# Kernel optimization log

Measured on AMD Instinct MI355X. Metric: run time of the kernel, lower is better.

Reference implementation:

```python
import jax, jax.numpy as jnp
import numpy as np

N = 100000
E = 1600000
G = 2048
D = 128
F_IN = 9
BN_EPS = 1e-5


def setup_inputs() -> dict:
    key = jax.random.key(0)
    ks = jax.random.split(key, 20)
    def glorot(k, shape):
        lim = float(np.sqrt(6.0 / (shape[0] + shape[1])))
        return jax.random.uniform(k, shape, jnp.float32, -lim, lim)
    inp = {
        'x': jax.random.normal(ks[0], (N, F_IN), jnp.float32),
        'edge_index': jax.random.randint(ks[1], (2, E), 0, N, jnp.int64),
        'batch_index': jnp.sort(jax.random.randint(ks[2], (N,), 0, G, jnp.int64)),
        'W0': glorot(ks[3], (F_IN, D)), 'b0': jnp.zeros((D,), jnp.float32),
        'W1': glorot(ks[4], (D, D)), 'b1': jnp.zeros((D,), jnp.float32),
        'W2': glorot(ks[5], (D, D)), 'b2': jnp.zeros((D,), jnp.float32),
        'W3': glorot(ks[6], (D, D)), 'b3': jnp.zeros((D,), jnp.float32),
        'g1': jnp.ones((D,), jnp.float32), 'be1': jnp.zeros((D,), jnp.float32),
        'g2': jnp.ones((D,), jnp.float32), 'be2': jnp.zeros((D,), jnp.float32),
        'g3': jnp.ones((D,), jnp.float32), 'be3': jnp.zeros((D,), jnp.float32),
        'Wout': glorot(ks[7], (D, 1)), 'bout': jnp.zeros((1,), jnp.float32),
    }
    return inp


def _gcn_conv(x, W, b, row, col, dinv):
    # PyG GCNConv: out = D^-1/2 (A+I) D^-1/2 (x W) + b
    lin = x @ W                                  # [N, D]
    coef = (dinv[row] * dinv[col])[:, None]      # [E, 1]
    agg = jax.ops.segment_sum(lin[row] * coef, col, num_segments=N)
    agg = agg + (dinv * dinv)[:, None] * lin     # self-loop term
    return agg + b


def _bn(x, gamma, beta):
    # BatchNorm1d training-mode: batch stats over node dim, biased variance
    m = jnp.mean(x, axis=0)
    v = jnp.var(x, axis=0)
    return (x - m) * jax.lax.rsqrt(v + BN_EPS) * gamma + beta


def reference(x, edge_index, batch_index, W0, b0, W1, b1, W2, b2, W3, b3,
              g1, be1, g2, be2, g3, be3, Wout, bout):
    row, col = edge_index[0], edge_index[1]
    # degrees with self-loops (all edge weights = 1)
    deg = jax.ops.segment_sum(jnp.ones((E,), x.dtype), col, num_segments=N) + 1.0
    dinv = jax.lax.rsqrt(deg)
    lrelu = lambda h: jax.nn.leaky_relu(h, negative_slope=0.01)

    h = _bn(lrelu(_gcn_conv(x, W0, b0, row, col, dinv)), g1, be1)
    h = _bn(lrelu(_gcn_conv(h, W1, b1, row, col, dinv)), g2, be2)
    h = _bn(lrelu(_gcn_conv(h, W2, b2, row, col, dinv)), g3, be3)
    h = lrelu(_gcn_conv(h, W3, b3, row, col, dinv))

    # global mean pool over graphs
    sums = jax.ops.segment_sum(h, batch_index, num_segments=G)
    cnts = jax.ops.segment_sum(jnp.ones((N,), x.dtype), batch_index, num_segments=G)
    pooled = sums / jnp.maximum(cnts, 1.0)[:, None]   # [G, D]
    return pooled @ Wout + bout                       # [G, 1]
```

## Files before the change

kernel.cpp:

```cpp
#include <hip/hip_runtime.h>


#define LRELU(z) ((z) > 0.f ? (z) : 0.01f * (z))
#define ADD4(d, s) \
  { d.x += s.x; d.y += s.y; d.z += s.z; d.w += s.w; }

typedef __attribute__((ext_vector_type(8))) short short8;
typedef __attribute__((ext_vector_type(4))) float float4v;

__device__ inline unsigned bf16_rn(float a) {
  unsigned u = __float_as_uint(a);
  return (u + 0x7FFFu + ((u >> 16) & 1u)) >> 16;
}

__device__ inline unsigned pack_bf16x2(float a, float b) {
  return bf16_rn(a) | (bf16_rn(b) << 16);
}

__device__ inline float bf16f(unsigned short s) {
  return __uint_as_float(((unsigned)s) << 16);
}

__device__ inline float4 unpack_bf16x4(uint2 u) {
  float4 r;
  r.x = __uint_as_float(u.x << 16);
  r.y = __uint_as_float(u.x & 0xffff0000u);
  r.z = __uint_as_float(u.y << 16);
  r.w = __uint_as_float(u.y & 0xffff0000u);
  return r;
}

__global__ __launch_bounds__(256) void k_count(const int* __restrict__ ei,
                                               int* __restrict__ cnt,
                                               int* __restrict__ rank, int E) {
  int i = blockIdx.x * 256 + threadIdx.x;
  if (i < E) rank[i] = atomicAdd(&cnt[ei[E + i]], 1);
}

__global__ __launch_bounds__(256) void k_scan1(const int* __restrict__ cnt,
                                               int* __restrict__ incl,
                                               int* __restrict__ bsums,
                                               float* __restrict__ dinv, int N) {
  __shared__ int s[256];
  int tid = threadIdx.x;
  int idx = blockIdx.x * 256 + tid;
  int v = (idx < N) ? cnt[idx] : 0;
  if (idx < N) dinv[idx] = rsqrtf((float)(v + 1));
  s[tid] = v;
  __syncthreads();
  for (int off = 1; off < 256; off <<= 1) {
    int t = (tid >= off) ? s[tid - off] : 0;
    __syncthreads();
    s[tid] += t;
    __syncthreads();
  }
  if (idx < N) incl[idx] = s[tid];
  if (tid == 255) bsums[blockIdx.x] = s[255];
}

__global__ __launch_bounds__(512) void k_scan2(const int* __restrict__ bsums,
                                               int* __restrict__ bpref, int nb) {
  __shared__ int s[512];
  int tid = threadIdx.x;
  int v = (tid < nb) ? bsums[tid] : 0;
  s[tid] = v;
  __syncthreads();
  for (int off = 1; off < 512; off <<= 1) {
    int t = (tid >= off) ? s[tid - off] : 0;
    __syncthreads();
    s[tid] += t;
    __syncthreads();
  }
  bpref[tid] = s[tid] - v;
}

__global__ __launch_bounds__(256) void k_cntg(const int* __restrict__ batch,
                                              float* __restrict__ cntG,
                                              int N, int G) {
  int g = blockIdx.x * 256 + threadIdx.x;
  if (g >= G) return;
  int lo = 0, hi = N;
  while (lo < hi) { int mid = (lo + hi) >> 1; if (batch[mid] < g) lo = mid + 1; else hi = mid; }
  int a = lo;
  hi = N;
  while (lo < hi) { int mid = (lo + hi) >> 1; if (batch[mid] < g + 1) lo = mid + 1; else hi = mid; }
  cntG[g] = (float)(lo - a);
}

__global__ __launch_bounds__(256) void k_scan3_prep(
    const int* __restrict__ incl, const int* __restrict__ cnt,
    const int* __restrict__ bpref, int* __restrict__ offs,
    int2* __restrict__ meta, const float* __restrict__ x,
    const float* __restrict__ dinv, unsigned* __restrict__ u, int N) {
  int idx = blockIdx.x * 256 + threadIdx.x;
  if (idx >= N) return;
  int c = cnt[idx];
  int off = incl[idx] - c + bpref[blockIdx.x];
  offs[idx] = off;
  meta[idx] = make_int2(off, c);
  float dv = dinv[idx];
  const float* xr = x + (size_t)idx * 9;
  unsigned p0 = pack_bf16x2(xr[0] * dv, xr[1] * dv);
  unsigned p1 = pack_bf16x2(xr[2] * dv, xr[3] * dv);
  unsigned p2 = pack_bf16x2(xr[4] * dv, xr[5] * dv);
  unsigned p3 = pack_bf16x2(xr[6] * dv, xr[7] * dv);
  unsigned p4 = pack_bf16x2(xr[8] * dv, dv);
  uint2* u2 = (uint2*)u;
  u2[(size_t)idx * 3 + 0] = make_uint2(p0, p1);
  u2[(size_t)idx * 3 + 1] = make_uint2(p2, p3);
  u2[(size_t)idx * 3 + 2] = make_uint2(p4, 0u);
}

__global__ __launch_bounds__(256) void k_csr(const int* __restrict__ ei,
                                             const int* __restrict__ offs,
                                             const int* __restrict__ rank,
                                             int* __restrict__ rows, int E) {
  int i = blockIdx.x * 256 + threadIdx.x;
  if (i < E) {
    int c = ei[E + i];
    rows[offs[c] + rank[i]] = ei[i];
  }
}

__global__ __launch_bounds__(256) void k_spmm9(
    const unsigned short* __restrict__ u, const int2* __restrict__ meta,
    const int* __restrict__ rows, const float* __restrict__ dinv,
    float* __restrict__ ax, float2* __restrict__ dq, int N) {
  const int t = threadIdx.x;
  const int g = t >> 4;
  const int f = t & 15;
  const int v = blockIdx.x * 16 + g;
  if (v >= N) return;
  const int2 m = meta[v];
  const int st = m.x;
  const int dg = m.y;
  const float dv = dinv[v];
  const bool act = (f < 10);
  float a0 = (f < 9) ? bf16f(u[(unsigned)v * 12u + f]) : 0.f;
  float a1 = 0.f, a2 = 0.f, a3 = 0.f;
  int idx = 0;
  if (f < (dg < 16 ? dg : 16)) idx = rows[st + f];
  for (int b = 0; b < dg; b += 16) {
    int rem = dg - b;
    int mm = rem < 16 ? rem : 16;
    const int cur = idx;
    if (b + 16 < dg) idx = (f < rem - 16) ? rows[st + b + 16 + f] : 0;
    int e = 0;
    for (; e + 8 <= mm; e += 8) {
      int r0 = __shfl(cur, e + 0, 16), r1 = __shfl(cur, e + 1, 16);
      int r2 = __shfl(cur, e + 2, 16), r3 = __shfl(cur, e + 3, 16);
      int r4 = __shfl(cur, e + 4, 16), r5 = __shfl(cur, e + 5, 16);
      int r6 = __shfl(cur, e + 6, 16), r7 = __shfl(cur, e + 7, 16);
      float x0 = 0, x1 = 0, x2 = 0, x3 = 0, x4 = 0, x5 = 0, x6 = 0, x7 = 0;
      if (act) {
        x0 = bf16f(u[(unsigned)r0 * 12u + f]); x1 = bf16f(u[(unsigned)r1 * 12u + f]);
        x2 = bf16f(u[(unsigned)r2 * 12u + f]); x3 = bf16f(u[(unsigned)r3 * 12u + f]);
        x4 = bf16f(u[(unsigned)r4 * 12u + f]); x5 = bf16f(u[(unsigned)r5 * 12u + f]);
        x6 = bf16f(u[(unsigned)r6 * 12u + f]); x7 = bf16f(u[(unsigned)r7 * 12u + f]);
      }
      a0 += x0; a1 += x1; a2 += x2; a3 += x3;
      a0 += x4; a1 += x5; a2 += x6; a3 += x7;
    }
    for (; e + 4 <= mm; e += 4) {
      int r0 = __shfl(cur, e + 0, 16), r1 = __shfl(cur, e + 1, 16);
      int r2 = __shfl(cur, e + 2, 16), r3 = __shfl(cur, e + 3, 16);
      float x0 = 0, x1 = 0, x2 = 0, x3 = 0;
      if (act) {
        x0 = bf16f(u[(unsigned)r0 * 12u + f]); x1 = bf16f(u[(unsigned)r1 * 12u + f]);
        x2 = bf16f(u[(unsigned)r2 * 12u + f]); x3 = bf16f(u[(unsigned)r3 * 12u + f]);
      }
      a0 += x0; a1 += x1; a2 += x2; a3 += x3;
    }
    for (; e < mm; e++) {
      int r = __shfl(cur, e, 16);
      if (act) a0 += bf16f(u[(unsigned)r * 12u + f]);
    }
  }
  float sum = (a0 + a1) + (a2 + a3);
  if (f < 9) {
    ax[(unsigned)v * 12u + f] = sum * dv;
  } else if (f == 9) {
    dq[v] = make_float2(dv, dv * (dv + sum));
  }
}

__global__ __launch_bounds__(256) void k_gemm_in(
    const float* __restrict__ ax, const float* __restrict__ W0,
    const float* __restrict__ b0, unsigned short* __restrict__ Abuf,
    float* __restrict__ stats, int N) {
  __shared__ float Wl[9 * 128];
  __shared__ float rs[128], rq[128];
  const int t = threadIdx.x;
  for (int i = t; i < 9 * 128; i += 256) Wl[i] = W0[i];
  if (t < 128) { rs[t] = 0.f; rq[t] = 0.f; }
  __syncthreads();
  const int col = t & 127;
  const int rsub = t >> 7;
  const int base = blockIdx.x * 16;
  const float bc = b0[col];
  float ls = 0.f, lq = 0.f;
  for (int it = 0; it < 8; it++) {
    int row = base + it * 2 + rsub;
    if (row < N) {
      const float* ar = ax + (size_t)row * 12;
      float acc = bc;
#pragma unroll
      for (int k = 0; k < 9; k++) acc += ar[k] * Wl[k * 128 + col];
      float a = LRELU(acc);
      Abuf[(size_t)row * 128 + col] = (unsigned short)bf16_rn(a);
      ls += a;
      lq += a * a;
    }
  }
  atomicAdd(&rs[col], ls);
  atomicAdd(&rq[col], lq);
  __syncthreads();
  if (t < 128) {
    atomicAdd(&stats[t], rs[t]);
    atomicAdd(&stats[128 + t], rq[t]);
  }
}

__global__ __launch_bounds__(256) void k_gemm_mfma(
    const unsigned short* __restrict__ Ab, const uint4* __restrict__ Wb,
    const float* __restrict__ dinv, unsigned short* __restrict__ Lb, int N) {
  __shared__ uint4 Bl[2048];
  __shared__ unsigned short Dl[4 * 2048];
  __shared__ float dvs[64];
  const int t = threadIdx.x;
  const int row0 = blockIdx.x * 64;
#pragma unroll
  for (int i = 0; i < 8; i++) Bl[t + i * 256] = Wb[t + i * 256];
  if (t < 64) {
    int r = row0 + t;
    dvs[t] = (r < N) ? dinv[r] : 0.f;
  }
  __syncthreads();
  const int w = t >> 6;
  const int lane = t & 63;
  const int m = lane & 15;
  const int quad = lane >> 4;
  const int rowA = min(row0 + w * 16 + m, N - 1);
  const uint4* Arow = (const uint4*)(Ab + (size_t)rowA * 128);
  uint4 a[4];
#pragma unroll
  for (int kt = 0; kt < 4; kt++) a[kt] = Arow[kt * 4 + quad];
  float4v acc[8];
#pragma unroll
  for (int nt = 0; nt < 8; nt++) acc[nt] = (float4v)0.0f;
#pragma unroll
  for (int nt = 0; nt < 8; nt++) {
#pragma unroll
    for (int kt = 0; kt < 4; kt++) {
      uint4 b = Bl[((kt * 8 + nt) * 4 + quad) * 16 + m];
      acc[nt] = __builtin_amdgcn_mfma_f32_16x16x32_bf16(
          *(short8*)&a[kt], *(short8*)&b, acc[nt], 0, 0, 0);
    }
  }
  unsigned short* Dw = Dl + w * 2048;
#pragma unroll
  for (int r = 0; r < 4; r++) {
    float dv = dvs[w * 16 + quad * 4 + r];
#pragma unroll
    for (int nt = 0; nt < 8; nt++) {
      Dw[(quad * 4 + r) * 128 + nt * 16 + m] =
          (unsigned short)bf16_rn(acc[nt][r] * dv);
    }
  }
  __syncthreads();
  const uint4* Dw4 = (const uint4*)Dw;
#pragma unroll
  for (int p = 0; p < 4; p++) {
    int row = row0 + w * 16 + p * 4 + (lane >> 4);
    if (row < N) {
      ((uint4*)(Lb + (size_t)row * 128))[lane & 15] = Dw4[p * 64 + lane];
    }
  }
}

__device__ inline float4 gacc32(const uint2* __restrict__ L2p,
                                const int* __restrict__ rows, uint2 self,
                                int st, int dg, int idx, int q32) {
  float4 s0 = unpack_bf16x4(self);
  float4 s1 = make_float4(0.f, 0.f, 0.f, 0.f), s2 = s1, s3 = s1;
  for (int b = 0; b < dg; b += 32) {
    int rem = dg - b;
    int mm = rem < 32 ? rem : 32;
    const int cur = idx;
    if (b + 32 < dg) idx = (q32 < rem - 32) ? rows[st + b + 32 + q32] : 0;
    int e = 0;
    for (; e + 8 <= mm; e += 8) {
      int r0 = __shfl(cur, e + 0, 32), r1 = __shfl(cur, e + 1, 32);
      int r2 = __shfl(cur, e + 2, 32), r3 = __shfl(cur, e + 3, 32);
      int r4 = __shfl(cur, e + 4, 32), r5 = __shfl(cur, e + 5, 32);
      int r6 = __shfl(cur, e + 6, 32), r7 = __shfl(cur, e + 7, 32);
      uint2 u0 = L2p[((unsigned)r0 << 5) + q32];
      uint2 u1 = L2p[((unsigned)r1 << 5) + q32];
      uint2 u2 = L2p[((unsigned)r2 << 5) + q32];
      uint2 u3 = L2p[((unsigned)r3 << 5) + q32];
      uint2 u4 = L2p[((unsigned)r4 << 5) + q32];
      uint2 u5 = L2p[((unsigned)r5 << 5) + q32];
      uint2 u6 = L2p[((unsigned)r6 << 5) + q32];
      uint2 u7 = L2p[((unsigned)r7 << 5) + q32];
      float4 g0 = unpack_bf16x4(u0); ADD4(s0, g0);
      float4 g1 = unpack_bf16x4(u1); ADD4(s1, g1);
      float4 g2 = unpack_bf16x4(u2); ADD4(s2, g2);
      float4 g3 = unpack_bf16x4(u3); ADD4(s3, g3);
      float4 g4 = unpack_bf16x4(u4); ADD4(s0, g4);
      float4 g5 = unpack_bf16x4(u5); ADD4(s1, g5);
      float4 g6 = unpack_bf16x4(u6); ADD4(s2, g6);
      float4 g7 = unpack_bf16x4(u7); ADD4(s3, g7);
    }
    for (; e + 4 <= mm; e += 4) {
      int r0 = __shfl(cur, e + 0, 32), r1 = __shfl(cur, e + 1, 32);
      int r2 = __shfl(cur, e + 2, 32), r3 = __shfl(cur, e + 3, 32);
      uint2 u0 = L2p[((unsigned)r0 << 5) + q32];
      uint2 u1 = L2p[((unsigned)r1 << 5) + q32];
      uint2 u2 = L2p[((unsigned)r2 << 5) + q32];
      uint2 u3 = L2p[((unsigned)r3 << 5) + q32];
      float4 g0 = unpack_bf16x4(u0); ADD4(s0, g0);
      float4 g1 = unpack_bf16x4(u1); ADD4(s1, g1);
      float4 g2 = unpack_bf16x4(u2); ADD4(s2, g2);
      float4 g3 = unpack_bf16x4(u3); ADD4(s3, g3);
    }
    for (; e < mm; e++) {
      int r = __shfl(cur, e, 32);
      float4 g0 = unpack_bf16x4(L2p[((unsigned)r << 5) + q32]);
      ADD4(s0, g0);
    }
  }
  float4 acc;
  acc.x = (s0.x + s1.x) + (s2.x + s3.x);
  acc.y = (s0.y + s1.y) + (s2.y + s3.y);
  acc.z = (s0.z + s1.z) + (s2.z + s3.z);
  acc.w = (s0.w + s1.w) + (s2.w + s3.w);
  return acc;
}

template <int MODE>
__global__ __launch_bounds__(256) void k_spmm(
    const unsigned* __restrict__ Lb, const int2* __restrict__ meta,
    const int* __restrict__ rows, const float2* __restrict__ dq,
    const float* __restrict__ tw, const float* __restrict__ bias,
    unsigned short* __restrict__ Aout, float* __restrict__ stats,
    const float* __restrict__ wout, const int* __restrict__ batch,
    float* __restrict__ pacc, int N) {
  const int t = threadIdx.x;
  const int g = t >> 5;
  const int q32 = t & 31;
  const uint2* __restrict__ L2p = (const uint2*)Lb;
  const float4 t4 = ((const float4*)tw)[q32];
  const float4 b4 = ((const float4*)bias)[q32];
  float4 wo4 = make_float4(0.f, 0.f, 0.f, 0.f);
  if (MODE == 1) wo4 = ((const float4*)wout)[q32];
  __shared__ float rs[128], rq[128];
  __shared__ float psum[16];
  __shared__ int pb[16];
  float4 ls = make_float4(0.f, 0.f, 0.f, 0.f), lq = ls;
  if (MODE == 0) {
    if (t < 128) { rs[t] = 0.f; rq[t] = 0.f; }
  } else {
    if (t < 16) pb[t] = -1;
  }
  __syncthreads();
  const int vb = blockIdx.x * 16 + g * 2;
  const bool ok0 = vb < N, ok1 = vb + 1 < N;
  const int v0 = ok0 ? vb : N - 1;
  const int v1 = ok1 ? vb + 1 : N - 1;
  const int2 m0 = meta[v0];
  const int2 m1 = meta[v1];
  const float2 dq0 = dq[v0];
  const float2 dq1 = dq[v1];
  uint2 self0 = L2p[((unsigned)v0 << 5) + q32];
  uint2 self1 = L2p[((unsigned)v1 << 5) + q32];
  int bt0 = 0, bt1 = 0;
  if (MODE == 1) { bt0 = batch[v0]; bt1 = batch[v1]; }
  int i0 = 0, i1 = 0;
  if (q32 < (m0.y < 32 ? m0.y : 32)) i0 = rows[m0.x + q32];
  if (q32 < (m1.y < 32 ? m1.y : 32)) i1 = rows[m1.x + q32];
  float4 acc0 = gacc32(L2p, rows, self0, m0.x, m0.y, i0, q32);
  float4 acc1 = gacc32(L2p, rows, self1, m1.x, m1.y, i1, q32);
  float4 a0, a1;
  a0.x = LRELU(dq0.x * acc0.x + dq0.y * t4.x + b4.x);
  a0.y = LRELU(dq0.x * acc0.y + dq0.y * t4.y + b4.y);
  a0.z = LRELU(dq0.x * acc0.z + dq0.y * t4.z + b4.z);
  a0.w = LRELU(dq0.x * acc0.w + dq0.y * t4.w + b4.w);
  a1.x = LRELU(dq1.x * acc1.x + dq1.y * t4.x + b4.x);
  a1.y = LRELU(dq1.x * acc1.y + dq1.y * t4.y + b4.y);
  a1.z = LRELU(dq1.x * acc1.z + dq1.y * t4.z + b4.z);
  a1.w = LRELU(dq1.x * acc1.w + dq1.y * t4.w + b4.w);
  if (MODE == 0) {
    if (ok0) {
      uint2 p;
      p.x = pack_bf16x2(a0.x, a0.y);
      p.y = pack_bf16x2(a0.z, a0.w);
      ((uint2*)Aout)[((unsigned)v0 << 5) + q32] = p;
      ls.x += a0.x; ls.y += a0.y; ls.z += a0.z; ls.w += a0.w;
      lq.x += a0.x * a0.x; lq.y += a0.y * a0.y;
      lq.z += a0.z * a0.z; lq.w += a0.w * a0.w;
    }
    if (ok1) {
      uint2 p;
      p.x = pack_bf16x2(a1.x, a1.y);
      p.y = pack_bf16x2(a1.z, a1.w);
      ((uint2*)Aout)[((unsigned)v1 << 5) + q32] = p;
      ls.x += a1.x; ls.y += a1.y; ls.z += a1.z; ls.w += a1.w;
      lq.x += a1.x * a1.x; lq.y += a1.y * a1.y;
      lq.z += a1.z * a1.z; lq.w += a1.w * a1.w;
    }
    const int f0 = q32 * 4;
    atomicAdd(&rs[f0 + 0], ls.x); atomicAdd(&rs[f0 + 1], ls.y);
    atomicAdd(&rs[f0 + 2], ls.z); atomicAdd(&rs[f0 + 3], ls.w);
    atomicAdd(&rq[f0 + 0], lq.x); atomicAdd(&rq[f0 + 1], lq.y);
    atomicAdd(&rq[f0 + 2], lq.z); atomicAdd(&rq[f0 + 3], lq.w);
    __syncthreads();
    if (t < 128) {
      atomicAdd(&stats[t], rs[t]);
      atomicAdd(&stats[128 + t], rq[t]);
    }
  } else {
    float sA = a0.x * wo4.x + a0.y * wo4.y + a0.z * wo4.z + a0.w * wo4.w;
    sA += __shfl_down(sA, 16, 32);
    sA += __shfl_down(sA, 8, 32);
    sA += __shfl_down(sA, 4, 32);
    sA += __shfl_down(sA, 2, 32);
    sA += __shfl_down(sA, 1, 32);
    float sB = a1.x * wo4.x + a1.y * wo4.y + a1.z * wo4.z + a1.w * wo4.w;
    sB += __shfl_down(sB, 16, 32);
    sB += __shfl_down(sB, 8, 32);
    sB += __shfl_down(sB, 4, 32);
    sB += __shfl_down(sB, 2, 32);
    sB += __shfl_down(sB, 1, 32);
    if (q32 == 0) {
      if (ok0) { psum[g * 2 + 0] = sA; pb[g * 2 + 0] = bt0; }
      if (ok1) { psum[g * 2 + 1] = sB; pb[g * 2 + 1] = bt1; }
    }
    __syncthreads();
    if (t < 16) {
      int b = pb[t];
      if (b >= 0 && (t == 0 || pb[t - 1] != b)) {
        float s = psum[t];
        for (int j = t + 1; j < 16 && pb[j] == b; j++) s += psum[j];
        atomicAdd(&pacc[b], s);
      }
    }
  }
}

__global__ __launch_bounds__(128) void k_fold(const float* __restrict__ stats,
                                              const float* __restrict__ g,
                                              const float* __restrict__ be,
                                              const float* __restrict__ W,
                                              unsigned short* __restrict__ Wb,
                                              float* __restrict__ tw, float invN) {
  const int j = threadIdx.x;
  const int i0 = blockIdx.x * 16;
  const int nt = j >> 4;
  const int n = j & 15;
  float acc = 0.f;
#pragma unroll
  for (int ii = 0; ii < 16; ii++) {
    int i = i0 + ii;
    float m = stats[i] * invN;
    float var = stats[128 + i] * invN - m * m;
    float si = g[i] * rsqrtf(var + 1e-5f);
    float ti = be[i] - m * si;
    float w = W[i * 128 + j];
    acc += ti * w;
    int kt = i >> 5, quad = (i >> 3) & 3, jj = i & 7;
    Wb[((((kt * 8 + nt) * 4 + quad) * 16 + n) << 3) + jj] =
        (unsigned short)bf16_rn(si * w);
  }
  atomicAdd(&tw[j], acc);
}

__global__ __launch_bounds__(256) void k_out(const float* __restrict__ pacc,
                                             const float* __restrict__ cntG,
                                             const float* __restrict__ bout,
                                             float* __restrict__ out, int G) {
  int i = blockIdx.x * 256 + threadIdx.x;
  if (i < G) out[i] = pacc[i] / fmaxf(cntG[i], 1.0f) + bout[0];
}

extern "C" void kernel_launch(void* const* d_in, const int* in_sizes, int n_in,
                              void* d_out, int out_size, void* d_ws, size_t ws_size,
                              hipStream_t stream) {
  const float* x    = (const float*)d_in[0];
  const int*   ei   = (const int*)d_in[1];
  const int*   batch= (const int*)d_in[2];
  const float* W0   = (const float*)d_in[3];
  const float* b0   = (const float*)d_in[4];
  const float* W1   = (const float*)d_in[5];
  const float* b1   = (const float*)d_in[6];
  const float* W2   = (const float*)d_in[7];
  const float* b2   = (const float*)d_in[8];
  const float* W3   = (const float*)d_in[9];
  const float* b3   = (const float*)d_in[10];
  const float* g1   = (const float*)d_in[11];
  const float* be1  = (const float*)d_in[12];
  const float* g2   = (const float*)d_in[13];
  const float* be2  = (const float*)d_in[14];
  const float* g3   = (const float*)d_in[15];
  const float* be3  = (const float*)d_in[16];
  const float* Wout = (const float*)d_in[17];
  const float* bout = (const float*)d_in[18];
  float* out = (float*)d_out;

  const int N = in_sizes[0] / 9;
  const int E = in_sizes[1] / 2;
  const int G = out_size;

  char* w = (char*)d_ws;
  auto alloc = [&](size_t bytes) -> void* {
    void* p = (void*)w;
    w += (bytes + 255) & ~(size_t)255;
    return p;
  };
  char* zbase = w;
  int*   cnt    = (int*)alloc((size_t)N * 4);
  float* pacc   = (float*)alloc((size_t)G * 4);
  float* stats  = (float*)alloc(3 * 256 * 4);
  float* tw3    = (float*)alloc(3 * 128 * 4);
  size_t zsize = (size_t)(w - zbase);
  int*   offs   = (int*)alloc((size_t)N * 4);
  int*   incl   = (int*)alloc((size_t)N * 4);
  int*   bsums  = (int*)alloc(512 * 4);
  int*   bpref  = (int*)alloc(512 * 4);
  float* dinv   = (float*)alloc((size_t)N * 4);
  float2* dq    = (float2*)alloc((size_t)N * 8);
  int2*  meta   = (int2*)alloc((size_t)N * 8);
  float* cntG   = (float*)alloc((size_t)G * 4);
  int*   rank   = (int*)alloc((size_t)E * 4);
  int*   rows   = (int*)alloc((size_t)E * 4);
  unsigned short* Wb = (unsigned short*)alloc(128 * 128 * 2);
  unsigned* u   = (unsigned*)alloc((size_t)N * 12 * 2);
  float* ax     = (float*)alloc((size_t)N * 12 * 4);
  unsigned* Lb  = (unsigned*)alloc((size_t)N * 128 * 2);
  unsigned short* Abuf = (unsigned short*)alloc((size_t)N * 128 * 2);

  hipMemsetAsync(zbase, 0, zsize, stream);

  const int eb  = (E + 255) / 256;
  const int nbN = (N + 255) / 256;
  const int sb  = (N + 15) / 16;
  const int mb  = (N + 63) / 64;
  const float invN = 1.0f / (float)N;
  float* twA = tw3;
  float* twB = tw3 + 128;
  float* twC = tw3 + 256;

  k_count<<<eb, 256, 0, stream>>>(ei, cnt, rank, E);
  k_scan1<<<nbN, 256, 0, stream>>>(cnt, incl, bsums, dinv, N);
  k_scan2<<<1, 512, 0, stream>>>(bsums, bpref, nbN);
  k_scan3_prep<<<nbN, 256, 0, stream>>>(incl, cnt, bpref, offs, meta, x, dinv, u, N);
  k_csr<<<eb, 256, 0, stream>>>(ei, offs, rank, rows, E);
  k_cntg<<<(G + 255) / 256, 256, 0, stream>>>(batch, cntG, N, G);

  k_spmm9<<<sb, 256, 0, stream>>>((const unsigned short*)u, meta, rows,
                                  dinv, ax, dq, N);
  k_gemm_in<<<sb, 256, 0, stream>>>(ax, W0, b0, Abuf, stats, N);
  k_fold<<<8, 128, 0, stream>>>(stats, g1, be1, W1, Wb, twA, invN);
  k_gemm_mfma<<<mb, 256, 0, stream>>>(Abuf, (const uint4*)Wb, dinv, (unsigned short*)Lb, N);
  k_spmm<0><<<sb, 256, 0, stream>>>(Lb, meta, rows, dq, twA, b1,
                                    Abuf, stats + 256, nullptr, nullptr, nullptr, N);
  k_fold<<<8, 128, 0, stream>>>(stats + 256, g2, be2, W2, Wb, twB, invN);
  k_gemm_mfma<<<mb, 256, 0, stream>>>(Abuf, (const uint4*)Wb, dinv, (unsigned short*)Lb, N);
  k_spmm<0><<<sb, 256, 0, stream>>>(Lb, meta, rows, dq, twB, b2,
                                    Abuf, stats + 512, nullptr, nullptr, nullptr, N);
  k_fold<<<8, 128, 0, stream>>>(stats + 512, g3, be3, W3, Wb, twC, invN);
  k_gemm_mfma<<<mb, 256, 0, stream>>>(Abuf, (const uint4*)Wb, dinv, (unsigned short*)Lb, N);
  k_spmm<1><<<sb, 256, 0, stream>>>(Lb, meta, rows, dq, twC, b3,
                                    nullptr, nullptr, Wout, batch, pacc, N);
  k_out<<<(G + 255) / 256, 256, 0, stream>>>(pacc, cntG, bout, out, G);
}
```

Baseline: 847.0 us.

## Quantize gathered features to int8 with per-column scales for SpMM

The GEMM kernel now tracks a per-column absolute maximum of its output. A new k_quant kernel converts the bf16 feature matrix into int8 using those scales. The sparse aggregation then gathers int8 neighbour rows, sums them in integers and rescales, while the self-loop term stays bf16. This halves the bytes moved by the edge gather, which should be the dominant memory cost. In exchange it adds an extra quantization pass and atomics per layer, and lowers aggregation precision, which risks accuracy tolerance.

```diff
diff --git a/kernel.cpp b/kernel.cpp
--- a/kernel.cpp
+++ b/kernel.cpp
@@ -2,8 +2,6 @@
 
 
 #define LRELU(z) ((z) > 0.f ? (z) : 0.01f * (z))
-#define ADD4(d, s) \
-  { d.x += s.x; d.y += s.y; d.z += s.z; d.w += s.w; }
 
 typedef __attribute__((ext_vector_type(8))) short short8;
 typedef __attribute__((ext_vector_type(4))) float float4v;
@@ -28,6 +26,13 @@
   r.z = __uint_as_float(u.y << 16);
   r.w = __uint_as_float(u.y & 0xffff0000u);
   return r;
+}
+
+__device__ inline void accb(int4& d, unsigned v) {
+  d.x += ((int)(v << 24)) >> 24;
+  d.y += ((int)(v << 16)) >> 24;
+  d.z += ((int)(v << 8)) >> 24;
+  d.w += ((int)v) >> 24;
 }
 
 __global__ __launch_bounds__(256) void k_count(const int* __restrict__ ei,
@@ -223,14 +228,17 @@
 
 __global__ __launch_bounds__(256) void k_gemm_mfma(
     const unsigned short* __restrict__ Ab, const uint4* __restrict__ Wb,
-    const float* __restrict__ dinv, unsigned short* __restrict__ Lb, int N) {
+    const float* __restrict__ dinv, unsigned short* __restrict__ Lb,
+    unsigned* __restrict__ colmaxU, int N) {
   __shared__ uint4 Bl[2048];
   __shared__ unsigned short Dl[4 * 2048];
   __shared__ float dvs[64];
+  __shared__ unsigned cmx[128];
   const int t = threadIdx.x;
   const int row0 = blockIdx.x * 64;
 #pragma unroll
   for (int i = 0; i < 8; i++) Bl[t + i * 256] = Wb[t + i * 256];
+  if (t < 128) cmx[t] = 0u;
   if (t < 64) {
     int r = row0 + t;
     dvs[t] = (r < N) ? dinv[r] : 0.f;
@@ -258,15 +266,22 @@
     }
   }
   unsigned short* Dw = Dl + w * 2048;
+  float cm8[8];
+#pragma unroll
+  for (int nt = 0; nt < 8; nt++) cm8[nt] = 0.f;
 #pragma unroll
   for (int r = 0; r < 4; r++) {
     float dv = dvs[w * 16 + quad * 4 + r];
 #pragma unroll
     for (int nt = 0; nt < 8; nt++) {
-      Dw[(quad * 4 + r) * 128 + nt * 16 + m] =
-          (unsigned short)bf16_rn(acc[nt][r] * dv);
-    }
-  }
+      float fv = acc[nt][r] * dv;
+      Dw[(quad * 4 + r) * 128 + nt * 16 + m] = (unsigned short)bf16_rn(fv);
+      cm8[nt] = fmaxf(cm8[nt], fabsf(fv));
+    }
+  }
+#pragma unroll
+  for (int nt = 0; nt < 8; nt++)
+    atomicMax(&cmx[nt * 16 + m], __float_as_uint(cm8[nt]));
   __syncthreads();
   const uint4* Dw4 = (const uint4*)Dw;
 #pragma unroll
@@ -276,13 +291,49 @@
       ((uint4*)(Lb + (size_t)row * 128))[lane & 15] = Dw4[p * 64 + lane];
     }
   }
-}
-
-__device__ inline float4 gacc32(const uint2* __restrict__ L2p,
-                                const int* __restrict__ rows, uint2 self,
-                                int st, int dg, int idx, int q32) {
-  float4 s0 = unpack_bf16x4(self);
-  float4 s1 = make_float4(0.f, 0.f, 0.f, 0.f), s2 = s1, s3 = s1;
+  if (t < 128) atomicMax(&colmaxU[t], cmx[t]);
+}
+
+__global__ __launch_bounds__(256) void k_quant(
+    const unsigned short* __restrict__ Lb, const unsigned* __restrict__ cmU,
+    unsigned* __restrict__ L8, int N4) {
+  __shared__ float invS[128];
+  const int t = threadIdx.x;
+  if (t < 128) {
+    float cm = __uint_as_float(cmU[t]);
+    invS[t] = cm > 0.f ? 127.f / cm : 0.f;
+  }
+  __syncthreads();
+  int idx = blockIdx.x * 256 + t;
+  if (idx >= N4) return;
+  const int row = idx >> 2;
+  const int seg = idx & 3;
+  const uint2* src = (const uint2*)(Lb + (size_t)row * 128 + seg * 32);
+  const float* inv = invS + seg * 32;
+  unsigned d[8];
+#pragma unroll
+  for (int j = 0; j < 8; j++) {
+    float4 f = unpack_bf16x4(src[j]);
+    int q0 = __float2int_rn(f.x * inv[j * 4 + 0]);
+    int q1 = __float2int_rn(f.y * inv[j * 4 + 1]);
+    int q2 = __float2int_rn(f.z * inv[j * 4 + 2]);
+    int q3 = __float2int_rn(f.w * inv[j * 4 + 3]);
+    q0 = max(-127, min(127, q0));
+    q1 = max(-127, min(127, q1));
+    q2 = max(-127, min(127, q2));
+    q3 = max(-127, min(127, q3));
+    d[j] = (unsigned)(q0 & 255) | ((unsigned)(q1 & 255) << 8) |
+           ((unsigned)(q2 & 255) << 16) | ((unsigned)(q3 & 255) << 24);
+  }
+  uint4* dst = (uint4*)((char*)L8 + (size_t)row * 128 + (size_t)seg * 32);
+  dst[0] = make_uint4(d[0], d[1], d[2], d[3]);
+  dst[1] = make_uint4(d[4], d[5], d[6], d[7]);
+}
+
+__device__ inline int4 gacci(const unsigned* __restrict__ L8d,
+                             const int* __restrict__ rows,
+                             int st, int dg, int idx, int q32) {
+  int4 s0 = make_int4(0, 0, 0, 0), s1 = s0, s2 = s0, s3 = s0;
   for (int b = 0; b < dg; b += 32) {
     int rem = dg - b;
     int mm = rem < 32 ? rem : 32;
@@ -294,42 +345,33 @@
       int r2 = __shfl(cur, e + 2, 32), r3 = __shfl(cur, e + 3, 32);
       int r4 = __shfl(cur, e + 4, 32), r5 = __shfl(cur, e + 5, 32);
       int r6 = __shfl(cur, e + 6, 32), r7 = __shfl(cur, e + 7, 32);
-      uint2 u0 = L2p[((unsigned)r0 << 5) + q32];
-      uint2 u1 = L2p[((unsigned)r1 << 5) + q32];
-      uint2 u2 = L2p[((unsigned)r2 << 5) + q32];
-      uint2 u3 = L2p[((unsigned)r3 << 5) + q32];
-      uint2 u4 = L2p[((unsigned)r4 << 5) + q32];
-      uint2 u5 = L2p[((unsigned)r5 << 5) + q32];
-      uint2 u6 = L2p[((unsigned)r6 << 5) + q32];
-      uint2 u7 = L2p[((unsigned)r7 << 5) + q32];
-      float4 g0 = unpack_bf16x4(u0); ADD4(s0, g0);
-      float4 g1 = unpack_bf16x4(u1); ADD4(s1, g1);
-      float4 g2 = unpack_bf16x4(u2); ADD4(s2, g2);
-      float4 g3 = unpack_bf16x4(u3); ADD4(s3, g3);
-      float4 g4 = unpack_bf16x4(u4); ADD4(s0, g4);
-      float4 g5 = unpack_bf16x4(u5); ADD4(s1, g5);
-      float4 g6 = unpack_bf16x4(u6); ADD4(s2, g6);
-      float4 g7 = unpack_bf16x4(u7); ADD4(s3, g7);
+      unsigned w0 = L8d[((unsigned)r0 << 5) + q32];
+      unsigned w1 = L8d[((unsigned)r1 << 5) + q32];
+      unsigned w2 = L8d[((unsigned)r2 << 5) + q32];
+      unsigned w3 = L8d[((unsigned)r3 << 5) + q32];
+      unsigned w4 = L8d[((unsigned)r4 << 5) + q32];
+      unsigned w5 = L8d[((unsigned)r5 << 5) + q32];
+      unsigned w6 = L8d[((unsigned)r6 << 5) + q32];
+      unsigned w7 = L8d[((unsigned)r7 << 5) + q32];
+      accb(s0, w0); accb(s1, w1); accb(s2, w2); accb(s3, w3);
+      accb(s0, w4); accb(s1, w5); accb(s2, w6); accb(s3, w7);
     }
     for (; e + 4 <= mm; e += 4) {
       int r0 = __shfl(cur, e + 0, 32), r1 = __shfl(cur, e + 1, 32);
       int r2 = __shfl(cur, e + 2, 32), r3 = __shfl(cur, e + 3, 32);
-      uint2 u0 = L2p[((unsigned)r0 << 5) + q32];
-      uint2 u1 = L2p[((unsigned)r1 << 5) + q32];
-      uint2 u2 = L2p[((unsigned)r2 << 5) + q32];
-      uint2 u3 = L2p[((unsigned)r3 << 5) + q32];
-      float4 g0 = unpack_bf16x4(u0); ADD4(s0, g0);
-      float4 g1 = unpack_bf16x4(u1); ADD4(s1, g1);
-      float4 g2 = unpack_bf16x4(u2); ADD4(s2, g2);
-      float4 g3 = unpack_bf16x4(u3); ADD4(s3, g3);
+      unsigned w0 = L8d[((unsigned)r0 << 5) + q32];
+      unsigned w1 = L8d[((unsigned)r1 << 5) + q32];
+      unsigned w2 = L8d[((unsigned)r2 << 5) + q32];
+      unsigned w3 = L8d[((unsigned)r3 << 5) + q32];
+      accb(s0, w0); accb(s1, w1); accb(s2, w2); accb(s3, w3);
     }
     for (; e < mm; e++) {
       int r = __shfl(cur, e, 32);
-      float4 g0 = unpack_bf16x4(L2p[((unsigned)r << 5) + q32]);
-      ADD4(s0, g0);
-    }
-  }
-  float4 acc;
+      unsigned w0 = L8d[((unsigned)r << 5) + q32];
+      accb(s0, w0);
+    }
+  }
+  int4 acc;
   acc.x = (s0.x + s1.x) + (s2.x + s3.x);
   acc.y = (s0.y + s1.y) + (s2.y + s3.y);
   acc.z = (s0.z + s1.z) + (s2.z + s3.z);
@@ -339,7 +381,8 @@
 
 template <int MODE>
 __global__ __launch_bounds__(256) void k_spmm(
-    const unsigned* __restrict__ Lb, const int2* __restrict__ meta,
+    const unsigned* __restrict__ Lb, const unsigned* __restrict__ L8d,
+    const unsigned* __restrict__ cmU, const int2* __restrict__ meta,
     const int* __restrict__ rows, const float2* __restrict__ dq,
     const float* __restrict__ tw, const float* __restrict__ bias,
     unsigned short* __restrict__ Aout, float* __restrict__ stats,
@@ -351,6 +394,9 @@
   const uint2* __restrict__ L2p = (const uint2*)Lb;
   const float4 t4 = ((const float4*)tw)[q32];
   const float4 b4 = ((const float4*)bias)[q32];
+  const float4 cm4 = ((const float4*)(const void*)cmU)[q32];
+  const float ksc = 1.f / 127.f;
+  const float4 s4 = make_float4(cm4.x * ksc, cm4.y * ksc, cm4.z * ksc, cm4.w * ksc);
   float4 wo4 = make_float4(0.f, 0.f, 0.f, 0.f);
   if (MODE == 1) wo4 = ((const float4*)wout)[q32];
   __shared__ float rs[128], rq[128];
@@ -378,8 +424,19 @@
   int i0 = 0, i1 = 0;
   if (q32 < (m0.y < 32 ? m0.y : 32)) i0 = rows[m0.x + q32];
   if (q32 < (m1.y < 32 ? m1.y : 32)) i1 = rows[m1.x + q32];
-  float4 acc0 = gacc32(L2p, rows, self0, m0.x, m0.y, i0, q32);
-  float4 acc1 = gacc32(L2p, rows, self1, m1.x, m1.y, i1, q32);
+  int4 ia0 = gacci(L8d, rows, m0.x, m0.y, i0, q32);
+  int4 ia1 = gacci(L8d, rows, m1.x, m1.y, i1, q32);
+  float4 sf0 = unpack_bf16x4(self0);
+  float4 sf1 = unpack_bf16x4(self1);
+  float4 acc0, acc1;
+  acc0.x = sf0.x + (float)ia0.x * s4.x;
+  acc0.y = sf0.y + (float)ia0.y * s4.y;
+  acc0.z = sf0.z + (float)ia0.z * s4.z;
+  acc0.w = sf0.w + (float)ia0.w * s4.w;
+  acc1.x = sf1.x + (float)ia1.x * s4.x;
+  acc1.y = sf1.y + (float)ia1.y * s4.y;
+  acc1.z = sf1.z + (float)ia1.z * s4.z;
+  acc1.w = sf1.w + (float)ia1.w * s4.w;
   float4 a0, a1;
   a0.x = LRELU(dq0.x * acc0.x + dq0.y * t4.x + b4.x);
   a0.y = LRELU(dq0.x * acc0.y + dq0.y * t4.y + b4.y);
@@ -521,6 +578,7 @@
   float* pacc   = (float*)alloc((size_t)G * 4);
   float* stats  = (float*)alloc(3 * 256 * 4);
   float* tw3    = (float*)alloc(3 * 128 * 4);
+  unsigned* cmU3 = (unsigned*)alloc(3 * 128 * 4);
   size_t zsize = (size_t)(w - zbase);
   int*   offs   = (int*)alloc((size_t)N * 4);
   int*   incl   = (int*)alloc((size_t)N * 4);
@@ -536,6 +594,7 @@
   unsigned* u   = (unsigned*)alloc((size_t)N * 12 * 2);
   float* ax     = (float*)alloc((size_t)N * 12 * 4);
   unsigned* Lb  = (unsigned*)alloc((size_t)N * 128 * 2);
+  unsigned* L8  = (unsigned*)alloc((size_t)N * 128);
   unsigned short* Abuf = (unsigned short*)alloc((size_t)N * 128 * 2);
 
   hipMemsetAsync(zbase, 0, zsize, stream);
@@ -544,10 +603,14 @@
   const int nbN = (N + 255) / 256;
   const int sb  = (N + 15) / 16;
   const int mb  = (N + 63) / 64;
+  const int qb  = (N * 4 + 255) / 256;
   const float invN = 1.0f / (float)N;
   float* twA = tw3;
   float* twB = tw3 + 128;
   float* twC = tw3 + 256;
+  unsigned* cmA = cmU3;
+  unsigned* cmB = cmU3 + 128;
+  unsigned* cmC = cmU3 + 256;
 
   k_count<<<eb, 256, 0, stream>>>(ei, cnt, rank, E);
   k_scan1<<<nbN, 256, 0, stream>>>(cnt, incl, bsums, dinv, N);
@@ -560,16 +623,24 @@
                                   dinv, ax, dq, N);
   k_gemm_in<<<sb, 256, 0, stream>>>(ax, W0, b0, Abuf, stats, N);
   k_fold<<<8, 128, 0, stream>>>(stats, g1, be1, W1, Wb, twA, invN);
-  k_gemm_mfma<<<mb, 256, 0, stream>>>(Abuf, (const uint4*)Wb, dinv, (unsigned short*)Lb, N);
-  k_spmm<0><<<sb, 256, 0, stream>>>(Lb, meta, rows, dq, twA, b1,
-                                    Abuf, stats + 256, nullptr, nullptr, nullptr, N);
+  k_gemm_mfma<<<mb, 256, 0, stream>>>(Abuf, (const uint4*)Wb, dinv,
+                                      (unsigned short*)Lb, cmA, N);
+  k_quant<<<qb, 256, 0, stream>>>((const unsigned short*)Lb, cmA, L8, N * 4);
+  k_spmm<0><<<sb, 256, 0, stream>>>(Lb, L8, cmA, meta, rows, dq, twA, b1,
+                                    Abuf, stats + 256, nullptr, nullptr,
+                                    nullptr, N);
   k_fold<<<8, 128, 0, stream>>>(stats + 256, g2, be2, W2, Wb, twB, invN);
-  k_gemm_mfma<<<mb, 256, 0, stream>>>(Abuf, (const uint4*)Wb, dinv, (unsigned short*)Lb, N);
-  k_spmm<0><<<sb, 256, 0, stream>>>(Lb, meta, rows, dq, twB, b2,
-                                    Abuf, stats + 512, nullptr, nullptr, nullptr, N);
+  k_gemm_mfma<<<mb, 256, 0, stream>>>(Abuf, (const uint4*)Wb, dinv,
+                                      (unsigned short*)Lb, cmB, N);
+  k_quant<<<qb, 256, 0, stream>>>((const unsigned short*)Lb, cmB, L8, N * 4);
+  k_spmm<0><<<sb, 256, 0, stream>>>(Lb, L8, cmB, meta, rows, dq, twB, b2,
+                                    Abuf, stats + 512, nullptr, nullptr,
+                                    nullptr, N);
   k_fold<<<8, 128, 0, stream>>>(stats + 512, g3, be3, W3, Wb, twC, invN);
-  k_gemm_mfma<<<mb, 256, 0, stream>>>(Abuf, (const uint4*)Wb, dinv, (unsigned short*)Lb, N);
-  k_spmm<1><<<sb, 256, 0, stream>>>(Lb, meta, rows, dq, twC, b3,
+  k_gemm_mfma<<<mb, 256, 0, stream>>>(Abuf, (const uint4*)Wb, dinv,
+                                      (unsigned short*)Lb, cmC, N);
+  k_quant<<<qb, 256, 0, stream>>>((const unsigned short*)Lb, cmC, L8, N * 4);
+  k_spmm<1><<<sb, 256, 0, stream>>>(Lb, L8, cmC, meta, rows, dq, twC, b3,
                                     nullptr, nullptr, Wout, batch, pacc, N);
   k_out<<<(G + 255) / 256, 256, 0, stream>>>(pacc, cntG, bout, out, G);
 }
```

Result: slower. 919.7 us (+8.6%).
